# Kernel optimization log

Hardware: AMD Instinct MI355X
Metric: run time of the kernel (lower is better)

## Reference

```python
import jax, jax.numpy as jnp
import numpy as np

N, D = 50000, 1000
FH1, FH2 = 256, 128
GH1, GH2, H = 64, 30, 3
NC = 10
E = 800000
BN_EPS = 1e-5


def setup_inputs() -> dict:
    key = jax.random.key(0)
    ks = iter(jax.random.split(key, 48))
    nk = lambda: next(ks)
    r = lambda *s: jax.random.normal(nk(), s, jnp.float32) * 0.05
    g = lambda n: 1.0 + jax.random.normal(nk(), (n,), jnp.float32) * 0.01
    return dict(
        x=jax.random.normal(nk(), (N, D), jnp.float32),
        edge_index=jax.random.randint(nk(), (2, E), 0, N, dtype=jnp.int32),
        enc_w1=r(D, FH1), enc_b1=r(FH1), enc_g1=g(FH1), enc_bt1=r(FH1),
        enc_w2=r(FH1, FH2), enc_b2=r(FH2), enc_g2=g(FH2), enc_bt2=r(FH2),
        gat1_w=r(FH2, H * GH1), gat1_asrc=r(H, GH1), gat1_adst=r(H, GH1), gat1_b=r(H * GH1),
        gat2_w=r(H * GH1, GH2), gat2_asrc=r(1, GH2), gat2_adst=r(1, GH2), gat2_b=r(GH2),
        gat3_w=r(H * GH1, GH2), gat3_asrc=r(1, GH2), gat3_adst=r(1, GH2), gat3_b=r(GH2),
        dec_w1=r(GH2, FH2), dec_b1=r(FH2), dec_g1=g(FH2), dec_bt1=r(FH2),
        dec_w2=r(FH2, FH1), dec_b2=r(FH1), dec_g2=g(FH1), dec_bt2=r(FH1),
        dec_w3=r(FH1, D), dec_b3=r(D),
        clu_w1=r(GH2, FH2), clu_b1=r(FH2), clu_g1=g(FH2), clu_bt1=r(FH2),
        clu_w2=r(FH2, NC), clu_b2=r(NC),
    )


def _bn_elu(h, w, b, gm, bt):
    # Linear -> BatchNorm1d (batch stats) -> ELU; dropout is identity at eval
    h = h @ w + b
    m = h.mean(0)
    v = h.var(0)
    return jax.nn.elu(gm * (h - m) * jax.lax.rsqrt(v + BN_EPS) + bt)


def _gat(h, src, dst, n, w, a_src, a_dst, b, heads, oc, concat):
    # PyG GATConv: per-head linear, edge-wise LeakyReLU(0.2) scores,
    # softmax over incoming edges of each dst node, weighted scatter-sum.
    hh = (h @ w).reshape(n, heads, oc)            # [N,H,C]
    s_src = jnp.sum(hh * a_src, -1)               # [N,H]
    s_dst = jnp.sum(hh * a_dst, -1)               # [N,H]
    e = jax.nn.leaky_relu(s_src[src] + s_dst[dst], negative_slope=0.2)  # [E,H]
    m = jax.ops.segment_max(e, dst, num_segments=n)
    p = jnp.exp(e - m[dst])
    denom = jax.ops.segment_sum(p, dst, num_segments=n)
    alpha = p / denom[dst]                        # [E,H]
    msg = hh[src] * alpha[..., None]              # [E,H,C]
    out = jax.ops.segment_sum(msg, dst, num_segments=n)
    out = out.reshape(n, heads * oc) if concat else out.mean(1)
    return out + b


def reference(x, edge_index,
              enc_w1, enc_b1, enc_g1, enc_bt1, enc_w2, enc_b2, enc_g2, enc_bt2,
              gat1_w, gat1_asrc, gat1_adst, gat1_b,
              gat2_w, gat2_asrc, gat2_adst, gat2_b,
              gat3_w, gat3_asrc, gat3_adst, gat3_b,
              dec_w1, dec_b1, dec_g1, dec_bt1, dec_w2, dec_b2, dec_g2, dec_bt2, dec_w3, dec_b3,
              clu_w1, clu_b1, clu_g1, clu_bt1, clu_w2, clu_b2):
    n = x.shape[0]
    loops = jnp.arange(n, dtype=edge_index.dtype)  # GATConv add_self_loops=True
    src = jnp.concatenate([edge_index[0], loops])
    dst = jnp.concatenate([edge_index[1], loops])

    h = _bn_elu(x, enc_w1, enc_b1, enc_g1, enc_bt1)
    h = _bn_elu(h, enc_w2, enc_b2, enc_g2, enc_bt2)
    h = jax.nn.relu(_gat(h, src, dst, n, gat1_w, gat1_asrc, gat1_adst, gat1_b, H, GH1, True))
    mu = _gat(h, src, dst, n, gat2_w, gat2_asrc, gat2_adst, gat2_b, 1, GH2, False)
    logvar = _gat(h, src, dst, n, gat3_w, gat3_asrc, gat3_adst, gat3_b, 1, GH2, False)
    z = mu  # eval-mode reparameterize returns mu

    d = _bn_elu(z, dec_w1, dec_b1, dec_g1, dec_bt1)
    d = _bn_elu(d, dec_w2, dec_b2, dec_g2, dec_bt2)
    x_rec = d @ dec_w3 + dec_b3

    c = _bn_elu(z, clu_w1, clu_b1, clu_g1, clu_bt1)
    pred = jax.nn.softmax(c @ clu_w2 + clu_b2, axis=1)
    return (pred, x_rec, z, mu, logvar)
```

## Files before the change

kernel.cpp:

```cpp
#include <hip/hip_runtime.h>
#include <hip/hip_bf16.h>

typedef short short8 __attribute__((ext_vector_type(8)));
typedef short short4v __attribute__((ext_vector_type(4)));
typedef float f32x4 __attribute__((ext_vector_type(4)));

static __device__ __forceinline__ short f2bf(float f){
  __hip_bfloat16 h = __float2bfloat16(f);
  return __builtin_bit_cast(short, h);
}
static __device__ __forceinline__ float b2f(short s){
  unsigned int u = ((unsigned int)(unsigned short)s) << 16;
  return __builtin_bit_cast(float, u);
}
static __device__ __forceinline__ float lrelu(float x){ return x > 0.f ? x : 0.2f*x; }
static __device__ __forceinline__ float eluf(float x){ return x > 0.f ? x : (__expf(x)-1.f); }
static __device__ __forceinline__ int imin(int a,int b){ return a<b?a:b; }

typedef const __attribute__((address_space(1))) void as1_void;
typedef __attribute__((address_space(3))) void as3_void;
static __device__ __forceinline__ void gload16(const void* g, void* l){
  __builtin_amdgcn_global_load_lds((as1_void*)g, (as3_void*)l, 16, 0, 0);
}
template<int NN> __device__ __forceinline__ void wait_vm(){
  if constexpr (NN==0) asm volatile("s_waitcnt vmcnt(0)" ::: "memory");
  else if constexpr (NN==3) asm volatile("s_waitcnt vmcnt(3)" ::: "memory");
  else if constexpr (NN==4) asm volatile("s_waitcnt vmcnt(4)" ::: "memory");
  else if constexpr (NN==6) asm volatile("s_waitcnt vmcnt(6)" ::: "memory");
  else if constexpr (NN==8) asm volatile("s_waitcnt vmcnt(8)" ::: "memory");
}

__global__ __launch_bounds__(256) void cvt_x(const float* __restrict__ x, short* __restrict__ xb, int M){
  int row = blockIdx.x*2 + (threadIdx.x>>7);
  int c8  = (threadIdx.x&127)*8;
  if (row >= M || c8 >= 1000) return;
  const float* p = x + (size_t)row*1000 + c8;
  float4 f0 = *(const float4*)p, f1 = *(const float4*)(p+4);
  short8 o;
  o[0]=f2bf(f0.x);o[1]=f2bf(f0.y);o[2]=f2bf(f0.z);o[3]=f2bf(f0.w);
  o[4]=f2bf(f1.x);o[5]=f2bf(f1.y);o[6]=f2bf(f1.z);o[7]=f2bf(f1.w);
  *(short8*)&xb[(size_t)row*1000 + c8] = o;
}

template<int BN, bool OBF16, bool CSTATS>
__global__ __launch_bounds__(256) void gemm_g(
    const short* __restrict__ A, int lda, const short* __restrict__ Bt, int ldb,
    void* __restrict__ Cv, const float* __restrict__ bias,
    float* __restrict__ ssum, float* __restrict__ ssq,
    int M, int N, int K, int ldc)
{
  constexpr int BM = 128, BK = 32, GPR = 4;
  constexpr int WN = BN/2, FM = 4, FN = WN/16;
  constexpr int AI = (BM*GPR)/(4*64);
  constexpr int BI_T = (BN*GPR)/64;
  constexpr bool BDUP = (BI_T < 4);
  constexpr int BI = BDUP ? BI_T : BI_T/4;
  constexpr int LPT = AI + BI;
  constexpr int TS = (BM+BN)*BK;
  __shared__ short lds[4][TS];

  const int tid = threadIdx.x, wid = tid>>6, lane = tid&63;
  const int wm = wid>>1, wn = wid&1;
  const int bm = blockIdx.x*BM, bn = blockIdx.y*BN;
  const int lr = lane&15, lg = lane>>4;
  const int nt = (K + BK - 1)/BK;

  f32x4 acc[FM][FN] = {};

  auto STAGE = [&](int t){
    int buf = t & 3, k0 = t*BK;
    #pragma unroll
    for (int i=0;i<AI;i++){
      int ci = wid*AI + i;
      int c = ci*64 + lane;
      int row = c>>2, g = c&3;
      int gr = imin(bm+row, M-1);
      const short* src = A + (size_t)gr*lda + k0 + ((g ^ (row&3))<<3);
      gload16(src, &lds[buf][ci*512]);
    }
    #pragma unroll
    for (int i=0;i<BI;i++){
      int bi = BDUP ? i : wid*BI + i;
      int c = bi*64 + lane;
      int row = c>>2, g = c&3;
      const short* src = Bt + (size_t)(bn+row)*ldb + k0 + ((g ^ (row&3))<<3);
      gload16(src, &lds[buf][BM*BK + bi*512]);
    }
  };

  for (int s=0; s<3 && s<nt; ++s) STAGE(s);

  for (int t=0; t<nt; ++t){
    int newer = imin(nt, t+3) - t - 1;
    if (newer >= 2) wait_vm<2*LPT>();
    else if (newer == 1) wait_vm<LPT>();
    else wait_vm<0>();
    __builtin_amdgcn_s_barrier();
    __builtin_amdgcn_sched_barrier(0);
    if (t+3 < nt) STAGE(t+3);
    int buf = t & 3;
    short8 af[FM], bf[FN];
    #pragma unroll
    for (int m=0;m<FM;m++){
      int r = wm*64 + m*16 + lr;
      af[m] = *(short8*)&lds[buf][r*BK + ((lg ^ (r&3))<<3)];
    }
    #pragma unroll
    for (int n=0;n<FN;n++){
      int r = wn*WN + n*16 + lr;
      bf[n] = *(short8*)&lds[buf][BM*BK + r*BK + ((lg ^ (r&3))<<3)];
    }
    #pragma unroll
    for (int m=0;m<FM;m++)
      #pragma unroll
      for (int n=0;n<FN;n++)
        acc[m][n] = __builtin_amdgcn_mfma_f32_16x16x32_bf16(af[m], bf[n], acc[m][n], 0, 0, 0);
  }

  #pragma unroll
  for (int m=0;m<FM;m++)
    #pragma unroll
    for (int n=0;n<FN;n++)
      #pragma unroll
      for (int q=0;q<4;q++){
        int row = bm + wm*64 + m*16 + lg*4 + q;
        int col = bn + wn*WN + n*16 + lr;
        if (row < M && col < N){
          float v = acc[m][n][q];
          if (bias) v += bias[col];
          if (OBF16) ((short*)Cv)[(size_t)row*ldc + col] = f2bf(v);
          else       ((float*)Cv)[(size_t)row*ldc + col] = v;
        }
      }
  if (CSTATS){
    #pragma unroll
    for (int n=0;n<FN;n++){
      float s = 0.f, q2 = 0.f;
      #pragma unroll
      for (int m=0;m<FM;m++)
        #pragma unroll
        for (int q=0;q<4;q++){
          int row = bm + wm*64 + m*16 + lg*4 + q;
          if (row < M){ float v = acc[m][n][q]; s += v; q2 += v*v; }
        }
      s  += __shfl_xor(s, 16);  s += __shfl_xor(s, 32);
      q2 += __shfl_xor(q2, 16); q2 += __shfl_xor(q2, 32);
      if (lg == 0){
        int col = bn + wn*WN + n*16 + lr;
        atomicAdd(&ssum[col], s);
        atomicAdd(&ssq[col],  q2);
      }
    }
  }
}

struct WEnt { const float* src; short* dst; int K, N, KP, NR; };
struct WTab { WEnt e[10]; };
__global__ __launch_bounds__(256) void wtrans_all(WTab tab){
  WEnt w = tab.e[blockIdx.y];
  int gid = blockIdx.x*256 + threadIdx.x;
  if (gid >= w.NR * w.KP) return;
  int n = gid / w.KP, k = gid - n*w.KP;
  float v = (k < w.K && n < w.N) ? w.src[(size_t)k*w.N + n] : 0.f;
  w.dst[gid] = f2bf(v);
}

template<int C>
__global__ __launch_bounds__(256) void bn_elu_apply2(const float* __restrict__ H, short* __restrict__ O,
    int M, float invM,
    const float* __restrict__ ssum, const float* __restrict__ ssq,
    const float* __restrict__ g, const float* __restrict__ bt){
  __shared__ float sc[C], sh[C];
  for (int c = threadIdx.x; c < C; c += 256){
    float mn  = ssum[c]*invM;
    float var = ssq[c]*invM - mn*mn;
    float s = g[c]*rsqrtf(var + 1e-5f);
    sc[c] = s; sh[c] = bt[c] - mn*s;
  }
  __syncthreads();
  int total4 = M*(C/4);
  for (int i = blockIdx.x*256+threadIdx.x; i < total4; i += gridDim.x*256){
    float4 v = ((const float4*)H)[i];
    int cb = (i*4) & (C-1);
    short4v o;
    o[0] = f2bf(eluf(v.x*sc[cb+0]+sh[cb+0]));
    o[1] = f2bf(eluf(v.y*sc[cb+1]+sh[cb+1]));
    o[2] = f2bf(eluf(v.z*sc[cb+2]+sh[cb+2]));
    o[3] = f2bf(eluf(v.w*sc[cb+3]+sh[cb+3]));
    ((short4v*)O)[i] = o;
  }
}

__global__ __launch_bounds__(256) void bn_elu_split(const float* __restrict__ H,
    short* __restrict__ Od, short* __restrict__ Oc, int M, float invM,
    const float* __restrict__ ssum, const float* __restrict__ ssq,
    const float* __restrict__ gd, const float* __restrict__ btd,
    const float* __restrict__ gc, const float* __restrict__ btc){
  __shared__ float sc[256], sh[256];
  {
    int c = threadIdx.x;
    float mn  = ssum[c]*invM;
    float var = ssq[c]*invM - mn*mn;
    float gg = (c<128) ? gd[c] : gc[c-128];
    float bb = (c<128) ? btd[c] : btc[c-128];
    float s = gg*rsqrtf(var + 1e-5f);
    sc[c] = s; sh[c] = bb - mn*s;
  }
  __syncthreads();
  int total4 = M*64;
  for (int i = blockIdx.x*256+threadIdx.x; i < total4; i += gridDim.x*256){
    float4 v = ((const float4*)H)[i];
    int cb = (i*4) & 255;
    short4v o;
    o[0] = f2bf(eluf(v.x*sc[cb+0]+sh[cb+0]));
    o[1] = f2bf(eluf(v.y*sc[cb+1]+sh[cb+1]));
    o[2] = f2bf(eluf(v.z*sc[cb+2]+sh[cb+2]));
    o[3] = f2bf(eluf(v.w*sc[cb+3]+sh[cb+3]));
    int row = i>>6;
    short* O = (cb < 128) ? Od : Oc;
    *(short4v*)&O[(size_t)row*128 + (cb&127)] = o;
  }
}

__global__ void hist_kernel(const int* __restrict__ d, int E, int* __restrict__ deg){
  int i = blockIdx.x*256 + threadIdx.x;
  if (i < E) atomicAdd(&deg[d[i]], 1);
}
__global__ __launch_bounds__(256) void scan1(const int* __restrict__ deg, int* __restrict__ offs,
                                             int* __restrict__ bsum, int n){
  __shared__ int sm[256];
  int tid = threadIdx.x;
  int base = blockIdx.x*1024 + tid*4;
  int v0 = base+0<n ? deg[base+0] : 0;
  int v1 = base+1<n ? deg[base+1] : 0;
  int v2 = base+2<n ? deg[base+2] : 0;
  int v3 = base+3<n ? deg[base+3] : 0;
  int ts = v0+v1+v2+v3;
  sm[tid] = ts;
  __syncthreads();
  #pragma unroll
  for (int d=1; d<256; d<<=1){
    int t = (tid>=d) ? sm[tid-d] : 0;
    __syncthreads();
    sm[tid] += t;
    __syncthreads();
  }
  int ex = sm[tid] - ts;
  if (base+0<n) offs[base+0] = ex;
  if (base+1<n) offs[base+1] = ex+v0;
  if (base+2<n) offs[base+2] = ex+v0+v1;
  if (base+3<n) offs[base+3] = ex+v0+v1+v2;
  if (tid==255) bsum[blockIdx.x] = sm[255];
}
__global__ __launch_bounds__(256) void scan3(int* __restrict__ offs, const int* __restrict__ bsum,
                      int* __restrict__ cursor, int n, int total){
  __shared__ int base_sm;
  int tgt = blockIdx.x >> 2;
  if (threadIdx.x < 64){
    int j = threadIdx.x;
    int v = (j < tgt) ? bsum[j] : 0;
    #pragma unroll
    for (int d=32; d; d>>=1) v += __shfl_xor(v, d);
    if (j == 0) base_sm = v;
  }
  __syncthreads();
  int i = blockIdx.x*256 + threadIdx.x;
  if (i < n){ int v = offs[i] + base_sm; offs[i]=v; cursor[i]=v; }
  if (i == 0) offs[n] = total;
}
__global__ void scatter_kernel(const int* __restrict__ s, const int* __restrict__ d, int E,
                               int* __restrict__ cursor, int* __restrict__ csr){
  int i = blockIdx.x*256 + threadIdx.x;
  if (i < E){ int pos = atomicAdd(&cursor[d[i]], 1); csr[pos] = s[i]; }
}

__global__ __launch_bounds__(256) void gat1_scores_bf(const short* __restrict__ hh,
    const float* __restrict__ as, const float* __restrict__ ad,
    float* __restrict__ ss, float* __restrict__ sd, int n){
  int w = threadIdx.x >> 6, lane = threadIdx.x & 63;
  int row = blockIdx.x*4 + w;
  if (row >= n) return;
  const short* hr = hh + (size_t)row*192;
  float ps[3], pd[3];
  #pragma unroll
  for (int h=0; h<3; h++){
    float v = b2f(hr[h*64 + lane]);
    ps[h] = v * as[h*64+lane];
    pd[h] = v * ad[h*64+lane];
  }
  #pragma unroll
  for (int m=32; m; m>>=1){
    #pragma unroll
    for (int h=0;h<3;h++){ ps[h] += __shfl_xor(ps[h], m); pd[h] += __shfl_xor(pd[h], m); }
  }
  if (lane == 0){
    #pragma unroll
    for (int h=0;h<3;h++){ ss[row*3+h]=ps[h]; sd[row*3+h]=pd[h]; }
  }
}

__global__ __launch_bounds__(256) void gat1_gather_bf(const int* __restrict__ offs, const int* __restrict__ csr,
    const short* __restrict__ hh, const float* __restrict__ ss, const float* __restrict__ sd,
    const float* __restrict__ bias, short* __restrict__ out, int n){
  int w = threadIdx.x >> 6, lane = threadIdx.x & 63;
  int dst = blockIdx.x*4 + w;
  if (dst >= n) return;
  float sd0 = sd[dst*3+0], sd1 = sd[dst*3+1], sd2 = sd[dst*3+2];
  float p0 = __expf(lrelu(ss[dst*3+0]+sd0));
  float p1 = __expf(lrelu(ss[dst*3+1]+sd1));
  float p2 = __expf(lrelu(ss[dst*3+2]+sd2));
  const short* hr = hh + (size_t)dst*192;
  float a0 = p0*b2f(hr[lane]), a1 = p1*b2f(hr[64+lane]), a2 = p2*b2f(hr[128+lane]);
  float d0 = p0, d1 = p1, d2 = p2;
  int p = offs[dst], pe = offs[dst+1];
  for (; p+4 <= pe; p += 4){
    int s0=csr[p], s1=csr[p+1], s2=csr[p+2], s3=csr[p+3];
    float e00=ss[s0*3+0], e01=ss[s0*3+1], e02=ss[s0*3+2];
    float e10=ss[s1*3+0], e11=ss[s1*3+1], e12=ss[s1*3+2];
    float e20=ss[s2*3+0], e21=ss[s2*3+1], e22=ss[s2*3+2];
    float e30=ss[s3*3+0], e31=ss[s3*3+1], e32=ss[s3*3+2];
    const short* r0 = hh + (size_t)s0*192;
    const short* r1 = hh + (size_t)s1*192;
    const short* r2 = hh + (size_t)s2*192;
    const short* r3 = hh + (size_t)s3*192;
    float v00=b2f(r0[lane]), v01=b2f(r0[64+lane]), v02=b2f(r0[128+lane]);
    float v10=b2f(r1[lane]), v11=b2f(r1[64+lane]), v12=b2f(r1[128+lane]);
    float v20=b2f(r2[lane]), v21=b2f(r2[64+lane]), v22=b2f(r2[128+lane]);
    float v30=b2f(r3[lane]), v31=b2f(r3[64+lane]), v32=b2f(r3[128+lane]);
    float q00=__expf(lrelu(e00+sd0)), q01=__expf(lrelu(e01+sd1)), q02=__expf(lrelu(e02+sd2));
    float q10=__expf(lrelu(e10+sd0)), q11=__expf(lrelu(e11+sd1)), q12=__expf(lrelu(e12+sd2));
    float q20=__expf(lrelu(e20+sd0)), q21=__expf(lrelu(e21+sd1)), q22=__expf(lrelu(e22+sd2));
    float q30=__expf(lrelu(e30+sd0)), q31=__expf(lrelu(e31+sd1)), q32=__expf(lrelu(e32+sd2));
    a0 += q00*v00 + q10*v10 + q20*v20 + q30*v30;
    a1 += q01*v01 + q11*v11 + q21*v21 + q31*v31;
    a2 += q02*v02 + q12*v12 + q22*v22 + q32*v32;
    d0 += q00+q10+q20+q30;
    d1 += q01+q11+q21+q31;
    d2 += q02+q12+q22+q32;
  }
  for (; p < pe; ++p){
    int src = csr[p];
    float q0 = __expf(lrelu(ss[src*3+0]+sd0));
    float q1 = __expf(lrelu(ss[src*3+1]+sd1));
    float q2 = __expf(lrelu(ss[src*3+2]+sd2));
    const short* sr = hh + (size_t)src*192;
    a0 += q0*b2f(sr[lane]); a1 += q1*b2f(sr[64+lane]); a2 += q2*b2f(sr[128+lane]);
    d0 += q0; d1 += q1; d2 += q2;
  }
  float v0 = a0/d0 + bias[lane];
  float v1 = a1/d1 + bias[64+lane];
  float v2 = a2/d2 + bias[128+lane];
  short* orow = out + (size_t)dst*192;
  orow[lane]      = f2bf(v0 > 0.f ? v0 : 0.f);
  orow[64+lane]   = f2bf(v1 > 0.f ? v1 : 0.f);
  orow[128+lane]  = f2bf(v2 > 0.f ? v2 : 0.f);
}

__global__ __launch_bounds__(256) void gat23_scores(const float* __restrict__ hh23,
    const float* __restrict__ a2s, const float* __restrict__ a2d,
    const float* __restrict__ a3s, const float* __restrict__ a3d,
    float* __restrict__ s2s, float* __restrict__ s2d, float* __restrict__ s3s, float* __restrict__ s3d, int n){
  int w = threadIdx.x >> 6, lane = threadIdx.x & 63;
  int row = blockIdx.x*4 + w;
  if (row >= n) return;
  float p[4] = {0.f,0.f,0.f,0.f};
  if (lane < 30){
    float v2 = hh23[(size_t)row*64+lane], v3 = hh23[(size_t)row*64+32+lane];
    p[0]=v2*a2s[lane]; p[1]=v2*a2d[lane]; p[2]=v3*a3s[lane]; p[3]=v3*a3d[lane];
  }
  #pragma unroll
  for (int m=32; m; m>>=1){
    #pragma unroll
    for (int j=0;j<4;j++) p[j] += __shfl_xor(p[j], m);
  }
  if (lane == 0){ s2s[row]=p[0]; s2d[row]=p[1]; s3s[row]=p[2]; s3d[row]=p[3]; }
}

__global__ __launch_bounds__(256) void gat23_gather(const int* __restrict__ offs, const int* __restrict__ csr,
    const float* __restrict__ hh23,
    const float* __restrict__ s2s, const float* __restrict__ s2d,
    const float* __restrict__ s3s, const float* __restrict__ s3d,
    const float* __restrict__ b2, const float* __restrict__ b3,
    float* __restrict__ zs, float* __restrict__ mus, float* __restrict__ lvs,
    short* __restrict__ zbf, int n){
  int w = threadIdx.x >> 6, lane = threadIdx.x & 63;
  int dst = blockIdx.x*4 + w;
  if (dst >= n) return;
  bool lo = lane < 32;
  int c = lane & 31;
  bool valid = c < 30;
  float sdA = s2d[dst], sdB = s3d[dst];
  float sdx = lo ? sdA : sdB;
  const float* ssx = lo ? s2s : s3s;
  float p2 = __expf(lrelu(s2s[dst]+sdA));
  float p3 = __expf(lrelu(s3s[dst]+sdB));
  float val = valid ? hh23[(size_t)dst*64+lane] : 0.f;
  float acc = (lo ? p2 : p3) * val;
  float den2 = p2, den3 = p3;
  int p = offs[dst], pe = offs[dst+1];
  for (; p+4 <= pe; p += 4){
    int s0=csr[p], s1=csr[p+1], s2i=csr[p+2], s3i=csr[p+3];
    float eA0=ssx[s0], eA1=ssx[s1], eA2=ssx[s2i], eA3=ssx[s3i];
    float f20=s2s[s0], f21=s2s[s1], f22=s2s[s2i], f23=s2s[s3i];
    float f30=s3s[s0], f31=s3s[s1], f32=s3s[s2i], f33=s3s[s3i];
    float v0 = valid ? hh23[(size_t)s0*64+lane] : 0.f;
    float v1 = valid ? hh23[(size_t)s1*64+lane] : 0.f;
    float v2 = valid ? hh23[(size_t)s2i*64+lane] : 0.f;
    float v3 = valid ? hh23[(size_t)s3i*64+lane] : 0.f;
    float qx0=__expf(lrelu(eA0+sdx)), qx1=__expf(lrelu(eA1+sdx));
    float qx2=__expf(lrelu(eA2+sdx)), qx3=__expf(lrelu(eA3+sdx));
    acc += qx0*v0 + qx1*v1 + qx2*v2 + qx3*v3;
    den2 += __expf(lrelu(f20+sdA)) + __expf(lrelu(f21+sdA)) + __expf(lrelu(f22+sdA)) + __expf(lrelu(f23+sdA));
    den3 += __expf(lrelu(f30+sdB)) + __expf(lrelu(f31+sdB)) + __expf(lrelu(f32+sdB)) + __expf(lrelu(f33+sdB));
  }
  for (; p < pe; ++p){
    int src = csr[p];
    float q2 = __expf(lrelu(s2s[src]+sdA));
    float q3 = __expf(lrelu(s3s[src]+sdB));
    float v = valid ? hh23[(size_t)src*64+lane] : 0.f;
    acc += (lo ? q2 : q3) * v;
    den2 += q2; den3 += q3;
  }
  if (lo){
    if (valid){
      float v = acc/den2 + b2[c];
      zs[(size_t)dst*30+c]  = v;
      mus[(size_t)dst*30+c] = v;
      zbf[(size_t)dst*32+c] = f2bf(v);
    } else {
      zbf[(size_t)dst*32+c] = 0;
    }
  } else if (valid){
    lvs[(size_t)dst*30+c] = acc/den3 + b3[c];
  }
}

__global__ __launch_bounds__(256) void softmax10(const float* __restrict__ in, float* __restrict__ out, int n){
  int row = blockIdx.x*256 + threadIdx.x;
  if (row >= n) return;
  const float* r = in + (size_t)row*10;
  float m = r[0];
  #pragma unroll
  for (int j=1;j<10;j++) m = fmaxf(m, r[j]);
  float e[10], s = 0.f;
  #pragma unroll
  for (int j=0;j<10;j++){ e[j] = __expf(r[j]-m); s += e[j]; }
  float inv = 1.f/s;
  float* o = out + (size_t)row*10;
  #pragma unroll
  for (int j=0;j<10;j++) o[j] = e[j]*inv;
}

static inline int cdiv(int a, int b){ return (a + b - 1) / b; }

extern "C" void kernel_launch(void* const* d_in, const int* in_sizes, int n_in,
                              void* d_out, int out_size, void* d_ws, size_t ws_size,
                              hipStream_t stream)
{
  const float* x        = (const float*)d_in[0];
  const int*   ei       = (const int*)  d_in[1];
  const float* enc_w1   = (const float*)d_in[2];
  const float* enc_g1   = (const float*)d_in[4];
  const float* enc_bt1  = (const float*)d_in[5];
  const float* enc_w2   = (const float*)d_in[6];
  const float* enc_g2   = (const float*)d_in[8];
  const float* enc_bt2  = (const float*)d_in[9];
  const float* gat1_w   = (const float*)d_in[10];
  const float* gat1_as  = (const float*)d_in[11];
  const float* gat1_ad  = (const float*)d_in[12];
  const float* gat1_b   = (const float*)d_in[13];
  const float* gat2_w   = (const float*)d_in[14];
  const float* gat2_as  = (const float*)d_in[15];
  const float* gat2_ad  = (const float*)d_in[16];
  const float* gat2_b   = (const float*)d_in[17];
  const float* gat3_w   = (const float*)d_in[18];
  const float* gat3_as  = (const float*)d_in[19];
  const float* gat3_ad  = (const float*)d_in[20];
  const float* gat3_b   = (const float*)d_in[21];
  const float* dec_w1   = (const float*)d_in[22];
  const float* dec_g1   = (const float*)d_in[24];
  const float* dec_bt1  = (const float*)d_in[25];
  const float* dec_w2   = (const float*)d_in[26];
  const float* dec_g2   = (const float*)d_in[28];
  const float* dec_bt2  = (const float*)d_in[29];
  const float* dec_w3   = (const float*)d_in[30];
  const float* dec_b3   = (const float*)d_in[31];
  const float* clu_w1   = (const float*)d_in[32];
  const float* clu_g1   = (const float*)d_in[34];
  const float* clu_bt1  = (const float*)d_in[35];
  const float* clu_w2   = (const float*)d_in[36];
  const float* clu_b2   = (const float*)d_in[37];

  const int N = in_sizes[0] / 1000;
  const int E = in_sizes[1] / 2;
  const int* e_src = ei;
  const int* e_dst = ei + E;
  const float invN = 1.f/(float)N;

  float* out  = (float*)d_out;
  float* pred = out;
  float* xrec = out + (size_t)N*10;
  float* zs   = xrec + (size_t)N*1000;
  float* mus  = zs  + (size_t)N*30;
  float* lvs  = mus + (size_t)N*30;

  char* ws = (char*)d_ws;
  size_t off = 0;
  auto alloc = [&](size_t bytes)->char*{
    char* p = ws + off;
    off = (off + bytes + 255) & ~(size_t)255;
    return p;
  };
  short* t_enc1  = (short*)alloc(256*1024*2);
  short* t_enc2  = (short*)alloc(128*256*2);
  short* t_gat1  = (short*)alloc(192*128*2);
  short* t_gat23 = (short*)alloc(64*192*2);
  short* t_dc1   = (short*)alloc(256*32*2);
  short* t_dec2  = (short*)alloc(256*128*2);
  short* t_dec3  = (short*)alloc(1024*256*2);
  short* t_clu2  = (short*)alloc(32*128*2);
  float* h1f  = (float*)alloc((size_t)N*256*4);
  short* h1b  = (short*)alloc((size_t)N*256*2);
  float* h2f  = (float*)alloc((size_t)N*128*4);
  short* h2b  = (short*)alloc((size_t)N*128*2);
  short* hh1b = (short*)alloc((size_t)N*192*2);
  short* h3b  = (short*)alloc((size_t)N*192*2);
  float* hh23f= (float*)alloc((size_t)N*64*4);
  short* zbf  = (short*)alloc((size_t)N*32*2);
  float* ss1  = (float*)alloc((size_t)N*3*4);
  float* sd1  = (float*)alloc((size_t)N*3*4);
  float* s2s  = (float*)alloc((size_t)N*4);
  float* s2d  = (float*)alloc((size_t)N*4);
  float* s3s  = (float*)alloc((size_t)N*4);
  float* s3d  = (float*)alloc((size_t)N*4);
  float* stats= (float*)alloc(2048*4);
  int*   deg  = (int*)alloc((size_t)(N+1)*4);
  int*   offs = (int*)alloc((size_t)(N+1)*4);
  int*   curp = (int*)alloc((size_t)(N+1)*4);
  int*   bsum = (int*)alloc(256*4);
  int*   csr  = (int*)alloc((size_t)E*4);
  short* xb   = h1b;
  float* dc1f = h2f;
  short* d1b  = h3b;
  short* c1b  = (short*)hh23f;
  float* d2f  = h1f;
  short* d2b  = h1b;
  float* c2   = (float*)zbf;
  float* st_enc1 = stats, *st_enc2 = stats+512, *st_dc1 = stats+768, *st_dec2 = stats+1280;

  WTab tab;
  tab.e[0] = {enc_w1, t_enc1, 1000, 256, 1024, 256};
  tab.e[1] = {enc_w2, t_enc2, 256, 128, 256, 128};
  tab.e[2] = {gat1_w, t_gat1, 128, 192, 128, 192};
  tab.e[3] = {gat2_w, t_gat23, 192, 30, 192, 32};
  tab.e[4] = {gat3_w, t_gat23 + 32*192, 192, 30, 192, 32};
  tab.e[5] = {dec_w1, t_dc1, 30, 128, 32, 128};
  tab.e[6] = {clu_w1, t_dc1 + 128*32, 30, 128, 32, 128};
  tab.e[7] = {dec_w2, t_dec2, 128, 256, 128, 256};
  tab.e[8] = {dec_w3, t_dec3, 256, 1000, 256, 1024};
  tab.e[9] = {clu_w2, t_clu2, 128, 10, 128, 32};
  wtrans_all<<<dim3(1024, 10), 256, 0, stream>>>(tab);
  hipMemsetAsync(stats, 0, 2048*4, stream);
  hipMemsetAsync(deg, 0, (size_t)(N+1)*4, stream);

  hist_kernel<<<cdiv(E,256), 256, 0, stream>>>(e_dst, E, deg);
  int nb = cdiv(N, 1024);
  scan1<<<nb, 256, 0, stream>>>(deg, offs, bsum, N);
  scan3<<<cdiv(N,256), 256, 0, stream>>>(offs, bsum, curp, N, E);
  scatter_kernel<<<cdiv(E,256), 256, 0, stream>>>(e_src, e_dst, E, curp, csr);

  const int MB = cdiv(N, 128);

  cvt_x<<<cdiv(N,2), 256, 0, stream>>>(x, xb, N);
  gemm_g<128,false,true><<<dim3(MB,2), 256, 0, stream>>>(xb, 1000, t_enc1, 1024, h1f, nullptr, st_enc1, st_enc1+256, N, 256, 1000, 256);
  bn_elu_apply2<256><<<2048, 256, 0, stream>>>(h1f, h1b, N, invN, st_enc1, st_enc1+256, enc_g1, enc_bt1);

  gemm_g<128,false,true><<<dim3(MB,1), 256, 0, stream>>>(h1b, 256, t_enc2, 256, h2f, nullptr, st_enc2, st_enc2+128, N, 128, 256, 128);
  bn_elu_apply2<128><<<2048, 256, 0, stream>>>(h2f, h2b, N, invN, st_enc2, st_enc2+128, enc_g2, enc_bt2);

  gemm_g<64,true,false><<<dim3(MB,3), 256, 0, stream>>>(h2b, 128, t_gat1, 128, hh1b, nullptr, nullptr, nullptr, N, 192, 128, 192);
  gat1_scores_bf<<<cdiv(N,4), 256, 0, stream>>>(hh1b, gat1_as, gat1_ad, ss1, sd1, N);
  gat1_gather_bf<<<cdiv(N,4), 256, 0, stream>>>(offs, csr, hh1b, ss1, sd1, gat1_b, h3b, N);

  gemm_g<64,false,false><<<dim3(MB,1), 256, 0, stream>>>(h3b, 192, t_gat23, 192, hh23f, nullptr, nullptr, nullptr, N, 64, 192, 64);
  gat23_scores<<<cdiv(N,4), 256, 0, stream>>>(hh23f, gat2_as, gat2_ad, gat3_as, gat3_ad, s2s, s2d, s3s, s3d, N);
  gat23_gather<<<cdiv(N,4), 256, 0, stream>>>(offs, csr, hh23f, s2s, s2d, s3s, s3d, gat2_b, gat3_b, zs, mus, lvs, zbf, N);

  gemm_g<128,false,true><<<dim3(MB,2), 256, 0, stream>>>(zbf, 32, t_dc1, 32, dc1f, nullptr, st_dc1, st_dc1+256, N, 256, 32, 256);
  bn_elu_split<<<2048, 256, 0, stream>>>(dc1f, d1b, c1b, N, invN, st_dc1, st_dc1+256, dec_g1, dec_bt1, clu_g1, clu_bt1);

  gemm_g<128,false,true><<<dim3(MB,2), 256, 0, stream>>>(d1b, 128, t_dec2, 128, d2f, nullptr, st_dec2, st_dec2+256, N, 256, 128, 256);
  bn_elu_apply2<256><<<2048, 256, 0, stream>>>(d2f, d2b, N, invN, st_dec2, st_dec2+256, dec_g2, dec_bt2);

  gemm_g<128,false,false><<<dim3(MB,8), 256, 0, stream>>>(d2b, 256, t_dec3, 256, xrec, dec_b3, nullptr, nullptr, N, 1000, 256, 1000);

  gemm_g<32,false,false><<<dim3(MB,1), 256, 0, stream>>>(c1b, 128, t_clu2, 128, c2, clu_b2, nullptr, nullptr, N, 10, 128, 10);
  softmax10<<<cdiv(N,256), 256, 0, stream>>>(c2, pred, N);
}
```

Before: 701.5 us.

## Replace GEMM with 512-thread BK=64 ring-buffered kernel and prefetch CSR indices

```diff
diff --git a/kernel.cpp b/kernel.cpp
--- a/kernel.cpp
+++ b/kernel.cpp
@@ -24,10 +24,11 @@
 }
 template<int NN> __device__ __forceinline__ void wait_vm(){
   if constexpr (NN==0) asm volatile("s_waitcnt vmcnt(0)" ::: "memory");
-  else if constexpr (NN==3) asm volatile("s_waitcnt vmcnt(3)" ::: "memory");
   else if constexpr (NN==4) asm volatile("s_waitcnt vmcnt(4)" ::: "memory");
   else if constexpr (NN==6) asm volatile("s_waitcnt vmcnt(6)" ::: "memory");
   else if constexpr (NN==8) asm volatile("s_waitcnt vmcnt(8)" ::: "memory");
+  else if constexpr (NN==12) asm volatile("s_waitcnt vmcnt(12)" ::: "memory");
+  else asm volatile("s_waitcnt vmcnt(0)" ::: "memory");
 }
 
 __global__ __launch_bounds__(256) void cvt_x(const float* __restrict__ x, short* __restrict__ xb, int M){
@@ -42,89 +43,84 @@
   *(short8*)&xb[(size_t)row*1000 + c8] = o;
 }
 
-template<int BN, bool OBF16, bool CSTATS>
-__global__ __launch_bounds__(256) void gemm_g(
+template<int BN, int BK, int RING, bool OBF16, bool CST>
+__global__ __launch_bounds__(512) void gemm_k(
     const short* __restrict__ A, int lda, const short* __restrict__ Bt, int ldb,
-    void* __restrict__ Cv, const float* __restrict__ bias,
-    float* __restrict__ ssum, float* __restrict__ ssq,
-    int M, int N, int K, int ldc)
+    void* __restrict__ Cv, int ldc, const float* __restrict__ bias,
+    int M, int N, int K,
+    float* __restrict__ o_sum, float* __restrict__ o_sq)
 {
-  constexpr int BM = 128, BK = 32, GPR = 4;
-  constexpr int WN = BN/2, FM = 4, FN = WN/16;
-  constexpr int AI = (BM*GPR)/(4*64);
-  constexpr int BI_T = (BN*GPR)/64;
-  constexpr bool BDUP = (BI_T < 4);
-  constexpr int BI = BDUP ? BI_T : BI_T/4;
-  constexpr int LPT = AI + BI;
-  constexpr int TS = (BM+BN)*BK;
-  __shared__ short lds[4][TS];
-
-  const int tid = threadIdx.x, wid = tid>>6, lane = tid&63;
-  const int wm = wid>>1, wn = wid&1;
-  const int bm = blockIdx.x*BM, bn = blockIdx.y*BN;
-  const int lr = lane&15, lg = lane>>4;
-  const int nt = (K + BK - 1)/BK;
-
-  f32x4 acc[FM][FN] = {};
-
-  auto STAGE = [&](int t){
-    int buf = t & 3, k0 = t*BK;
-    #pragma unroll
-    for (int i=0;i<AI;i++){
-      int ci = wid*AI + i;
-      int c = ci*64 + lane;
-      int row = c>>2, g = c&3;
-      int gr = imin(bm+row, M-1);
-      const short* src = A + (size_t)gr*lda + k0 + ((g ^ (row&3))<<3);
-      gload16(src, &lds[buf][ci*512]);
-    }
-    #pragma unroll
-    for (int i=0;i<BI;i++){
-      int bi = BDUP ? i : wid*BI + i;
-      int c = bi*64 + lane;
-      int row = c>>2, g = c&3;
-      const short* src = Bt + (size_t)(bn+row)*ldb + k0 + ((g ^ (row&3))<<3);
-      gload16(src, &lds[buf][BM*BK + bi*512]);
-    }
-  };
-
-  for (int s=0; s<3 && s<nt; ++s) STAGE(s);
-
-  for (int t=0; t<nt; ++t){
-    int newer = imin(nt, t+3) - t - 1;
-    if (newer >= 2) wait_vm<2*LPT>();
-    else if (newer == 1) wait_vm<LPT>();
-    else wait_vm<0>();
-    __builtin_amdgcn_s_barrier();
-    __builtin_amdgcn_sched_barrier(0);
-    if (t+3 < nt) STAGE(t+3);
-    int buf = t & 3;
-    short8 af[FM], bf[FN];
-    #pragma unroll
-    for (int m=0;m<FM;m++){
-      int r = wm*64 + m*16 + lr;
-      af[m] = *(short8*)&lds[buf][r*BK + ((lg ^ (r&3))<<3)];
-    }
+  constexpr int BM=128, GPR=BK/8, RPC=64/GPR;
+  constexpr int AI=(BM/RPC)/8, BI=(BN/RPC)/8;
+  constexpr int LPT=AI+BI, DEPTH=RING-1;
+  constexpr int WN=BN/2, FM=2, FN=WN/16, NKK=BK/32;
+  static_assert(RING==2 || RING==3, "ring");
+  __shared__ short lds[RING][(BM+BN)*BK];
+
+  const int tid=threadIdx.x, wid=tid>>6, lane=tid&63;
+  const int wm=wid>>1, wn=wid&1;
+  const int bm=blockIdx.x*BM, bn=blockIdx.y*BN;
+  const int lr=lane&15, lg=lane>>4;
+  const int nt=(K+BK-1)/BK;
+  const int l_g = lane & (GPR-1), l_r = lane / GPR;
+  f32x4 acc[FM][FN]={};
+
+  #define STG(T,S) do{ if((T)<nt){ int k0_=(T)*BK;                          \
+    _Pragma("unroll") for(int i_=0;i_<AI;i_++){                             \
+      int ci_=wid*AI+i_; int row_=ci_*RPC+l_r;                              \
+      int g_=l_g^(row_&(GPR-1));                                            \
+      gload16(A+(size_t)imin(bm+row_,M-1)*lda+k0_+g_*8, (void*)&lds[S][ci_*512]); } \
+    _Pragma("unroll") for(int i_=0;i_<BI;i_++){                             \
+      int bi_=wid*BI+i_; int row_=bi_*RPC+l_r;                              \
+      int g_=l_g^(row_&(GPR-1));                                            \
+      gload16(Bt+(size_t)(bn+row_)*ldb+k0_+g_*8, (void*)&lds[S][BM*BK+bi_*512]); } \
+  }}while(0)
+
+  #define CMP(S) do{                                                        \
+    _Pragma("unroll") for(int kk_=0;kk_<NKK;kk_++){                         \
+      short8 af_[FM], bf_[FN];                                              \
+      _Pragma("unroll") for(int m_=0;m_<FM;m_++){                           \
+        int r_=wm*32+m_*16+lr;                                              \
+        af_[m_]=*(short8*)&lds[S][r_*BK+((kk_*4+lg)^(r_&(GPR-1)))*8]; }     \
+      _Pragma("unroll") for(int n_=0;n_<FN;n_++){                           \
+        int r_=wn*WN+n_*16+lr;                                              \
+        bf_[n_]=*(short8*)&lds[S][BM*BK+r_*BK+((kk_*4+lg)^(r_&(GPR-1)))*8]; } \
+      _Pragma("unroll") for(int m_=0;m_<FM;m_++)                            \
+        _Pragma("unroll") for(int n_=0;n_<FN;n_++)                          \
+          acc[m_][n_]=__builtin_amdgcn_mfma_f32_16x16x32_bf16(af_[m_],bf_[n_],acc[m_][n_],0,0,0); \
+  }}while(0)
+
+  #define BODYK(T,S) do{ if((T)<nt){                                        \
+    int newer_=imin(nt,(T)+DEPTH)-(T)-1;                                    \
+    if(DEPTH>=2 && newer_>=2) wait_vm<2*LPT>();                             \
+    else if(newer_>=1) wait_vm<LPT>();                                      \
+    else wait_vm<0>();                                                      \
+    __builtin_amdgcn_s_barrier();                                           \
+    __builtin_amdgcn_sched_barrier(0);                                      \
+    STG((T)+DEPTH,((S)+DEPTH)%RING);                                        \
+    CMP(S);                                                                 \
+  }}while(0)
+
+  STG(0,0);
+  if (DEPTH>=2) STG(1,1);
+  for (int t=0;t<nt;t+=RING){
+    BODYK(t+0,0);
+    BODYK(t+1,1);
+    if constexpr (RING>=3) BODYK(t+2,2);
+  }
+  #undef STG
+  #undef CMP
+  #undef BODYK
+
+  const int rowb = bm + wm*32 + lg*4;
+  #pragma unroll
+  for (int m=0;m<FM;m++)
     #pragma unroll
     for (int n=0;n<FN;n++){
-      int r = wn*WN + n*16 + lr;
-      bf[n] = *(short8*)&lds[buf][BM*BK + r*BK + ((lg ^ (r&3))<<3)];
-    }
-    #pragma unroll
-    for (int m=0;m<FM;m++)
-      #pragma unroll
-      for (int n=0;n<FN;n++)
-        acc[m][n] = __builtin_amdgcn_mfma_f32_16x16x32_bf16(af[m], bf[n], acc[m][n], 0, 0, 0);
-  }
-
-  #pragma unroll
-  for (int m=0;m<FM;m++)
-    #pragma unroll
-    for (int n=0;n<FN;n++)
+      int col = bn + wn*WN + n*16 + lr;
       #pragma unroll
       for (int q=0;q<4;q++){
-        int row = bm + wm*64 + m*16 + lg*4 + q;
-        int col = bn + wn*WN + n*16 + lr;
+        int row = rowb + m*16 + q;
         if (row < M && col < N){
           float v = acc[m][n][q];
           if (bias) v += bias[col];
@@ -132,7 +128,8 @@
           else       ((float*)Cv)[(size_t)row*ldc + col] = v;
         }
       }
-  if (CSTATS){
+    }
+  if (CST){
     #pragma unroll
     for (int n=0;n<FN;n++){
       float s = 0.f, q2 = 0.f;
@@ -140,22 +137,21 @@
       for (int m=0;m<FM;m++)
         #pragma unroll
         for (int q=0;q<4;q++){
-          int row = bm + wm*64 + m*16 + lg*4 + q;
+          int row = rowb + m*16 + q;
           if (row < M){ float v = acc[m][n][q]; s += v; q2 += v*v; }
         }
       s  += __shfl_xor(s, 16);  s += __shfl_xor(s, 32);
       q2 += __shfl_xor(q2, 16); q2 += __shfl_xor(q2, 32);
       if (lg == 0){
         int col = bn + wn*WN + n*16 + lr;
-        atomicAdd(&ssum[col], s);
-        atomicAdd(&ssq[col],  q2);
+        if (col < N){ atomicAdd(&o_sum[col], s); atomicAdd(&o_sq[col], q2); }
       }
     }
   }
 }
 
 struct WEnt { const float* src; short* dst; int K, N, KP, NR; };
-struct WTab { WEnt e[10]; };
+struct WTab { WEnt e[12]; };
 __global__ __launch_bounds__(256) void wtrans_all(WTab tab){
   WEnt w = tab.e[blockIdx.y];
   int gid = blockIdx.x*256 + threadIdx.x;
@@ -313,8 +309,12 @@
   float a0 = p0*b2f(hr[lane]), a1 = p1*b2f(hr[64+lane]), a2 = p2*b2f(hr[128+lane]);
   float d0 = p0, d1 = p1, d2 = p2;
   int p = offs[dst], pe = offs[dst+1];
-  for (; p+4 <= pe; p += 4){
-    int s0=csr[p], s1=csr[p+1], s2=csr[p+2], s3=csr[p+3];
+  int n0=0,n1=0,n2=0,n3=0;
+  if (p+4 <= pe){ n0=csr[p]; n1=csr[p+1]; n2=csr[p+2]; n3=csr[p+3]; }
+  while (p+4 <= pe){
+    int s0=n0, s1=n1, s2=n2, s3=n3;
+    int pn = p+4;
+    if (pn+4 <= pe){ n0=csr[pn]; n1=csr[pn+1]; n2=csr[pn+2]; n3=csr[pn+3]; }
     float e00=ss[s0*3+0], e01=ss[s0*3+1], e02=ss[s0*3+2];
     float e10=ss[s1*3+0], e11=ss[s1*3+1], e12=ss[s1*3+2];
     float e20=ss[s2*3+0], e21=ss[s2*3+1], e22=ss[s2*3+2];
@@ -337,6 +337,7 @@
     d0 += q00+q10+q20+q30;
     d1 += q01+q11+q21+q31;
     d2 += q02+q12+q22+q32;
+    p = pn;
   }
   for (; p < pe; ++p){
     int src = csr[p];
@@ -398,8 +399,12 @@
   float acc = (lo ? p2 : p3) * val;
   float den2 = p2, den3 = p3;
   int p = offs[dst], pe = offs[dst+1];
-  for (; p+4 <= pe; p += 4){
-    int s0=csr[p], s1=csr[p+1], s2i=csr[p+2], s3i=csr[p+3];
+  int n0=0,n1=0,n2=0,n3=0;
+  if (p+4 <= pe){ n0=csr[p]; n1=csr[p+1]; n2=csr[p+2]; n3=csr[p+3]; }
+  while (p+4 <= pe){
+    int s0=n0, s1=n1, s2i=n2, s3i=n3;
+    int pn = p+4;
+    if (pn+4 <= pe){ n0=csr[pn]; n1=csr[pn+1]; n2=csr[pn+2]; n3=csr[pn+3]; }
     float eA0=ssx[s0], eA1=ssx[s1], eA2=ssx[s2i], eA3=ssx[s3i];
     float f20=s2s[s0], f21=s2s[s1], f22=s2s[s2i], f23=s2s[s3i];
     float f30=s3s[s0], f31=s3s[s1], f32=s3s[s2i], f33=s3s[s3i];
@@ -412,6 +417,7 @@
     acc += qx0*v0 + qx1*v1 + qx2*v2 + qx3*v3;
     den2 += __expf(lrelu(f20+sdA)) + __expf(lrelu(f21+sdA)) + __expf(lrelu(f22+sdA)) + __expf(lrelu(f23+sdA));
     den3 += __expf(lrelu(f30+sdB)) + __expf(lrelu(f31+sdB)) + __expf(lrelu(f32+sdB)) + __expf(lrelu(f33+sdB));
+    p = pn;
   }
   for (; p < pe; ++p){
     int src = csr[p];
@@ -426,12 +432,13 @@
       float v = acc/den2 + b2[c];
       zs[(size_t)dst*30+c]  = v;
       mus[(size_t)dst*30+c] = v;
-      zbf[(size_t)dst*32+c] = f2bf(v);
+      zbf[(size_t)dst*64+c] = f2bf(v);
     } else {
-      zbf[(size_t)dst*32+c] = 0;
+      zbf[(size_t)dst*64+c] = 0;
     }
-  } else if (valid){
-    lvs[(size_t)dst*30+c] = acc/den3 + b3[c];
+  } else {
+    if (valid) lvs[(size_t)dst*30+c] = acc/den3 + b3[c];
+    zbf[(size_t)dst*64+32+c] = 0;
   }
 }
 
@@ -513,12 +520,12 @@
   };
   short* t_enc1  = (short*)alloc(256*1024*2);
   short* t_enc2  = (short*)alloc(128*256*2);
-  short* t_gat1  = (short*)alloc(192*128*2);
-  short* t_gat23 = (short*)alloc(64*192*2);
-  short* t_dc1   = (short*)alloc(256*32*2);
+  short* t_gat1  = (short*)alloc(256*128*2);
+  short* t_gat23 = (short*)alloc(128*192*2);
+  short* t_dc1   = (short*)alloc(256*64*2);
   short* t_dec2  = (short*)alloc(256*128*2);
   short* t_dec3  = (short*)alloc(1024*256*2);
-  short* t_clu2  = (short*)alloc(32*128*2);
+  short* t_clu2  = (short*)alloc(128*128*2);
   float* h1f  = (float*)alloc((size_t)N*256*4);
   short* h1b  = (short*)alloc((size_t)N*256*2);
   float* h2f  = (float*)alloc((size_t)N*128*4);
@@ -526,7 +533,7 @@
   short* hh1b = (short*)alloc((size_t)N*192*2);
   short* h3b  = (short*)alloc((size_t)N*192*2);
   float* hh23f= (float*)alloc((size_t)N*64*4);
-  short* zbf  = (short*)alloc((size_t)N*32*2);
+  short* zbf  = (short*)alloc((size_t)N*64*2);
   float* ss1  = (float*)alloc((size_t)N*3*4);
   float* sd1  = (float*)alloc((size_t)N*3*4);
   float* s2s  = (float*)alloc((size_t)N*4);
@@ -549,17 +556,19 @@
   float* st_enc1 = stats, *st_enc2 = stats+512, *st_dc1 = stats+768, *st_dec2 = stats+1280;
 
   WTab tab;
-  tab.e[0] = {enc_w1, t_enc1, 1000, 256, 1024, 256};
-  tab.e[1] = {enc_w2, t_enc2, 256, 128, 256, 128};
-  tab.e[2] = {gat1_w, t_gat1, 128, 192, 128, 192};
-  tab.e[3] = {gat2_w, t_gat23, 192, 30, 192, 32};
-  tab.e[4] = {gat3_w, t_gat23 + 32*192, 192, 30, 192, 32};
-  tab.e[5] = {dec_w1, t_dc1, 30, 128, 32, 128};
-  tab.e[6] = {clu_w1, t_dc1 + 128*32, 30, 128, 32, 128};
-  tab.e[7] = {dec_w2, t_dec2, 128, 256, 128, 256};
-  tab.e[8] = {dec_w3, t_dec3, 256, 1000, 256, 1024};
-  tab.e[9] = {clu_w2, t_clu2, 128, 10, 128, 32};
-  wtrans_all<<<dim3(1024, 10), 256, 0, stream>>>(tab);
+  tab.e[0]  = {enc_w1, t_enc1, 1000, 256, 1024, 256};
+  tab.e[1]  = {enc_w2, t_enc2, 256, 128, 256, 128};
+  tab.e[2]  = {gat1_w, t_gat1, 128, 192, 128, 256};
+  tab.e[3]  = {gat2_w, t_gat23, 192, 30, 192, 32};
+  tab.e[4]  = {gat3_w, t_gat23 + 32*192, 192, 30, 192, 32};
+  tab.e[5]  = {gat2_w, t_gat23 + 64*192, 192, 0, 192, 64};
+  tab.e[6]  = {dec_w1, t_dc1, 30, 128, 64, 128};
+  tab.e[7]  = {clu_w1, t_dc1 + 128*64, 30, 128, 64, 128};
+  tab.e[8]  = {dec_w2, t_dec2, 128, 256, 128, 256};
+  tab.e[9]  = {dec_w3, t_dec3, 256, 1000, 256, 1024};
+  tab.e[10] = {clu_w2, t_clu2, 128, 10, 128, 128};
+  tab.e[11] = {enc_w1, t_enc1, 0, 0, 0, 0};
+  wtrans_all<<<dim3(1024, 12), 256, 0, stream>>>(tab);
   hipMemsetAsync(stats, 0, 2048*4, stream);
   hipMemsetAsync(deg, 0, (size_t)(N+1)*4, stream);
 
@@ -572,28 +581,36 @@
   const int MB = cdiv(N, 128);
 
   cvt_x<<<cdiv(N,2), 256, 0, stream>>>(x, xb, N);
-  gemm_g<128,false,true><<<dim3(MB,2), 256, 0, stream>>>(xb, 1000, t_enc1, 1024, h1f, nullptr, st_enc1, st_enc1+256, N, 256, 1000, 256);
+  gemm_k<256,64,3,false,true><<<dim3(MB,1), 512, 0, stream>>>(
+      xb, 1000, t_enc1, 1024, h1f, 256, nullptr, N, 256, 1000, st_enc1, st_enc1+256);
   bn_elu_apply2<256><<<2048, 256, 0, stream>>>(h1f, h1b, N, invN, st_enc1, st_enc1+256, enc_g1, enc_bt1);
 
-  gemm_g<128,false,true><<<dim3(MB,1), 256, 0, stream>>>(h1b, 256, t_enc2, 256, h2f, nullptr, st_enc2, st_enc2+128, N, 128, 256, 128);
+  gemm_k<128,64,2,false,true><<<dim3(MB,1), 512, 0, stream>>>(
+      h1b, 256, t_enc2, 256, h2f, 128, nullptr, N, 128, 256, st_enc2, st_enc2+128);
   bn_elu_apply2<128><<<2048, 256, 0, stream>>>(h2f, h2b, N, invN, st_enc2, st_enc2+128, enc_g2, enc_bt2);
 
-  gemm_g<64,true,false><<<dim3(MB,3), 256, 0, stream>>>(h2b, 128, t_gat1, 128, hh1b, nullptr, nullptr, nullptr, N, 192, 128, 192);
+  gemm_k<128,64,2,true,false><<<dim3(MB,2), 512, 0, stream>>>(
+      h2b, 128, t_gat1, 128, hh1b, 192, nullptr, N, 192, 128, nullptr, nullptr);
   gat1_scores_bf<<<cdiv(N,4), 256, 0, stream>>>(hh1b, gat1_as, gat1_ad, ss1, sd1, N);
   gat1_gather_bf<<<cdiv(N,4), 256, 0, stream>>>(offs, csr, hh1b, ss1, sd1, gat1_b, h3b, N);
 
-  gemm_g<64,false,false><<<dim3(MB,1), 256, 0, stream>>>(h3b, 192, t_gat23, 192, hh23f, nullptr, nullptr, nullptr, N, 64, 192, 64);
+  gemm_k<128,64,2,false,false><<<dim3(MB,1), 512, 0, stream>>>(
+      h3b, 192, t_gat23, 192, hh23f, 64, nullptr, N, 64, 192, nullptr, nullptr);
   gat23_scores<<<cdiv(N,4), 256, 0, stream>>>(hh23f, gat2_as, gat2_ad, gat3_as, gat3_ad, s2s, s2d, s3s, s3d, N);
   gat23_gather<<<cdiv(N,4), 256, 0, stream>>>(offs, csr, hh23f, s2s, s2d, s3s, s3d, gat2_b, gat3_b, zs, mus, lvs, zbf, N);
 
-  gemm_g<128,false,true><<<dim3(MB,2), 256, 0, stream>>>(zbf, 32, t_dc1, 32, dc1f, nullptr, st_dc1, st_dc1+256, N, 256, 32, 256);
+  gemm_k<128,64,2,false,true><<<dim3(MB,2), 512, 0, stream>>>(
+      zbf, 64, t_dc1, 64, dc1f, 256, nullptr, N, 256, 32, st_dc1, st_dc1+256);
   bn_elu_split<<<2048, 256, 0, stream>>>(dc1f, d1b, c1b, N, invN, st_dc1, st_dc1+256, dec_g1, dec_bt1, clu_g1, clu_bt1);
 
-  gemm_g<128,false,true><<<dim3(MB,2), 256, 0, stream>>>(d1b, 128, t_dec2, 128, d2f, nullptr, st_dec2, st_dec2+256, N, 256, 128, 256);
+  gemm_k<128,64,2,false,true><<<dim3(MB,2), 512, 0, stream>>>(
+      d1b, 128, t_dec2, 128, d2f, 256, nullptr, N, 256, 128, st_dec2, st_dec2+256);
   bn_elu_apply2<256><<<2048, 256, 0, stream>>>(d2f, d2b, N, invN, st_dec2, st_dec2+256, dec_g2, dec_bt2);
 
-  gemm_g<128,false,false><<<dim3(MB,8), 256, 0, stream>>>(d2b, 256, t_dec3, 256, xrec, dec_b3, nullptr, nullptr, N, 1000, 256, 1000);
-
-  gemm_g<32,false,false><<<dim3(MB,1), 256, 0, stream>>>(c1b, 128, t_clu2, 128, c2, clu_b2, nullptr, nullptr, N, 10, 128, 10);
+  gemm_k<128,64,2,false,false><<<dim3(MB,8), 512, 0, stream>>>(
+      d2b, 256, t_dec3, 256, xrec, 1000, dec_b3, N, 1000, 256, nullptr, nullptr);
+
+  gemm_k<128,64,2,false,false><<<dim3(MB,1), 512, 0, stream>>>(
+      c1b, 128, t_clu2, 128, c2, 10, clu_b2, N, 10, 128, nullptr, nullptr);
   softmax10<<<cdiv(N,256), 256, 0, stream>>>(c2, pred, N);
 }
```

Result: slower. 734.0 us (+4.6%).
